# Optimization experiments

Hardware: AMD Instinct MI355X
Metric: run time of the kernel (lower is better)

## Reference

```python
import jax, jax.numpy as jnp
import numpy as np

EPS = 1e-08

def setup_inputs() -> dict:
    key = jax.random.key(0)
    ks = jax.random.split(key, 6)
    B, IN_C, OUT_C, H, W, STYLE_DIM = 16, 64, 64, 128, 128, 512
    x = jax.random.normal(ks[0], (B, IN_C, H, W), dtype=jnp.float32)
    style = jax.random.normal(ks[1], (B, STYLE_DIM), dtype=jnp.float32)
    # weight: (1, out_c, in_c, ks, ks) with kernel_size=1, kaiming-like scale
    fan_in = IN_C * 1 * 1
    gain = np.sqrt(2.0 / (1.0 + 0.2 ** 2))
    weight = jax.random.normal(ks[2], (1, OUT_C, IN_C, 1, 1), dtype=jnp.float32) * (gain / np.sqrt(fan_in))
    bias = jnp.zeros((1, OUT_C), dtype=jnp.float32)
    # geo_feature: Linear(style_dim, in_c)
    geo_w = jax.random.normal(ks[3], (IN_C, STYLE_DIM), dtype=jnp.float32) * (np.sqrt(2.0 / (1.0 + 0.2 ** 2)) / np.sqrt(STYLE_DIM))
    geo_b = jnp.zeros((IN_C,), dtype=jnp.float32)
    return {"x": x, "style": style, "weight": weight, "bias": bias, "geo_w": geo_w, "geo_b": geo_b}

def reference(x, style, weight, bias, geo_w, geo_b):
    # x: (b, in_c, h, w); style: (b, style_dim)
    # geo_feature linear -> (b, in_c), modulation factor (style + 1)
    s = style @ geo_w.T + geo_b                      # (b, in_c)
    mod = s + 1.0
    # per-sample modulated weight: (b, out_c, in_c, 1, 1) -> (b, out_c, in_c)
    w = weight[:, :, :, 0, 0] * mod[:, None, :]       # (b, out_c, in_c)
    # demodulate over (in_c, kh, kw)
    demod = jax.lax.rsqrt(jnp.sum(w * w, axis=2) + EPS)  # (b, out_c)
    w = w * demod[:, :, None]
    # groups=batch 1x1 conv == per-sample channel mixing
    out = jnp.einsum('boi,bihw->bohw', w, x)          # (b, out_c, h, w)
    out = out + bias[0][None, :, None, None]
    return out
```

## Files before the change

kernel.cpp:

```cpp
#include <hip/hip_runtime.h>
#include <hip/hip_bf16.h>

#define B_SZ 16
#define IN_C 64
#define OUT_C 64
#define STYLE_DIM 512
#define HW 16384
#define HWT 256
#define EPS 1e-8f

__global__ __launch_bounds__(256) void fused_kernel(
    const float* __restrict__ x,
    const float* __restrict__ style,
    const float* __restrict__ weight,
    const float* __restrict__ bias,
    const float* __restrict__ geo_w,
    const float* __restrict__ geo_b,
    float* __restrict__ out)
{
    __shared__ float smod[IN_C];
    __shared__ float sWT[IN_C * OUT_C];
    __shared__ float xs0[8][HWT];
    __shared__ float xs1[8][HWT];

    const int tid  = threadIdx.x;
    const int b    = blockIdx.x >> 6;
    const int hwt  = (blockIdx.x & 63) * HWT;
    const int wv   = tid >> 6;
    const int lane = tid & 63;

    const float* xg0 = x + ((size_t)b * IN_C + 2 * wv) * HW + hwt + lane * 4;

#define STAGE(CH, XS) do {                                                   \
        __builtin_amdgcn_global_load_lds(                                    \
            (const __attribute__((address_space(1))) void*)(xg0 + (size_t)(CH) * 8 * HW),        \
            (__attribute__((address_space(3))) void*)&(XS)[2 * wv][0], 16, 0, 0);                \
        __builtin_amdgcn_global_load_lds(                                    \
            (const __attribute__((address_space(1))) void*)(xg0 + ((size_t)(CH) * 8 + 1) * HW),  \
            (__attribute__((address_space(3))) void*)&(XS)[2 * wv + 1][0], 16, 0, 0);            \
    } while (0)

    STAGE(0, xs0);

    {
        const int i    = tid >> 2;
        const int part = tid & 3;
        const float4* st4 = reinterpret_cast<const float4*>(style + b * STYLE_DIM + part * 128);
        const float4* gw4 = reinterpret_cast<const float4*>(geo_w + i * STYLE_DIM + part * 128);
        float s = 0.0f;
        #pragma unroll
        for (int k = 0; k < 32; ++k) {
            const float4 a = st4[k];
            const float4 g = gw4[k];
            s = fmaf(a.x, g.x, s); s = fmaf(a.y, g.y, s);
            s = fmaf(a.z, g.z, s); s = fmaf(a.w, g.w, s);
        }
        s += __shfl_xor(s, 1);
        s += __shfl_xor(s, 2);
        if (part == 0) smod[i] = s + geo_b[i] + 1.0f;
    }
    __syncthreads();

    {
        const int o    = tid >> 2;
        const int part = tid & 3;
        const float* wr = weight + o * IN_C + part * 16;
        const float* sm = smod + part * 16;
        float wvv[16];
        float d = 0.0f;
        #pragma unroll
        for (int k = 0; k < 16; ++k) {
            wvv[k] = wr[k] * sm[k];
            d = fmaf(wvv[k], wvv[k], d);
        }
        d += __shfl_xor(d, 1);
        d += __shfl_xor(d, 2);
        d = rsqrtf(d + EPS);
        #pragma unroll
        for (int k = 0; k < 16; ++k)
            sWT[(part * 16 + k) * OUT_C + o] = wvv[k] * d;
    }
    __syncthreads();

    const int og  = (tid >> 5) * 8;
    const int hwg = (tid & 31) * 4;

    float acc[8][8];
    #pragma unroll
    for (int o = 0; o < 8; ++o)
        #pragma unroll
        for (int h = 0; h < 8; ++h) acc[o][h] = 0.0f;

#define COMPUTE_CHUNK(XS, C0) do {                                           \
        _Pragma("unroll")                                                    \
        for (int cc = 0; cc < 8; ++cc) {                                     \
            const float4 xa = *reinterpret_cast<const float4*>(&(XS)[cc][hwg]);        \
            const float4 xc = *reinterpret_cast<const float4*>(&(XS)[cc][128 + hwg]);  \
            const float4 w0 = *reinterpret_cast<const float4*>(&sWT[((C0) + cc) * OUT_C + og]);     \
            const float4 w1 = *reinterpret_cast<const float4*>(&sWT[((C0) + cc) * OUT_C + og + 4]); \
            const float wvv[8] = {w0.x, w0.y, w0.z, w0.w, w1.x, w1.y, w1.z, w1.w};     \
            const float xv[8]  = {xa.x, xa.y, xa.z, xa.w, xc.x, xc.y, xc.z, xc.w};     \
            _Pragma("unroll")                                                \
            for (int o = 0; o < 8; ++o)                                      \
                _Pragma("unroll")                                            \
                for (int h = 0; h < 8; ++h)                                  \
                    acc[o][h] = fmaf(wvv[o], xv[h], acc[o][h]);              \
        }                                                                    \
    } while (0)

    #pragma unroll
    for (int cp = 0; cp < 4; ++cp) {
        const int cA = 2 * cp, cB = 2 * cp + 1;
        STAGE(cB, xs1);
        COMPUTE_CHUNK(xs0, cA * 8);
        __syncthreads();
        if (cB < 7) STAGE(cB + 1, xs0);
        COMPUTE_CHUNK(xs1, cB * 8);
        if (cB < 7) __syncthreads();
    }
#undef COMPUTE_CHUNK
#undef STAGE

    float* ob = out + ((size_t)b * OUT_C + og) * HW + hwt;
    #pragma unroll
    for (int o = 0; o < 8; ++o) {
        const float bv = bias[og + o];
        float4 r0, r1;
        r0.x = acc[o][0] + bv;  r0.y = acc[o][1] + bv;
        r0.z = acc[o][2] + bv;  r0.w = acc[o][3] + bv;
        r1.x = acc[o][4] + bv;  r1.y = acc[o][5] + bv;
        r1.z = acc[o][6] + bv;  r1.w = acc[o][7] + bv;
        *reinterpret_cast<float4*>(ob + (size_t)o * HW + hwg)       = r0;
        *reinterpret_cast<float4*>(ob + (size_t)o * HW + 128 + hwg) = r1;
    }
}

extern "C" void kernel_launch(void* const* d_in, const int* in_sizes, int n_in,
                              void* d_out, int out_size, void* d_ws, size_t ws_size,
                              hipStream_t stream) {
    const float* x      = (const float*)d_in[0];
    const float* style  = (const float*)d_in[1];
    const float* weight = (const float*)d_in[2];
    const float* bias   = (const float*)d_in[3];
    const float* geo_w  = (const float*)d_in[4];
    const float* geo_b  = (const float*)d_in[5];
    float* out = (float*)d_out;

    fused_kernel<<<B_SZ * (HW / HWT), 256, 0, stream>>>(
        x, style, weight, bias, geo_w, geo_b, out);
}
```

Baseline: 152.8 us.

## Split weight modulation into separate kernel and stream x directly from global

Moves the per-sample modulated weight computation into a small precursor kernel that writes transposed weights to workspace. The conv kernel drops LDS staging and barriers, loading x directly with float2 prefetch and wave-uniform weights, with fewer accumulators per thread for higher occupancy. It adds a second launch, and the waves of each block re-read x through cache.

Measured after the change: 275.6 us. 1.8x slower.

```diff
diff --git a/kernel.cpp b/kernel.cpp
--- a/kernel.cpp
+++ b/kernel.cpp
@@ -6,41 +6,18 @@
 #define OUT_C 64
 #define STYLE_DIM 512
 #define HW 16384
-#define HWT 256
 #define EPS 1e-8f
 
-__global__ __launch_bounds__(256) void fused_kernel(
-    const float* __restrict__ x,
+__global__ __launch_bounds__(256) void modw_kernel(
     const float* __restrict__ style,
     const float* __restrict__ weight,
-    const float* __restrict__ bias,
     const float* __restrict__ geo_w,
     const float* __restrict__ geo_b,
-    float* __restrict__ out)
+    float* __restrict__ WT)
 {
+    const int b   = blockIdx.x;
+    const int tid = threadIdx.x;
     __shared__ float smod[IN_C];
-    __shared__ float sWT[IN_C * OUT_C];
-    __shared__ float xs0[8][HWT];
-    __shared__ float xs1[8][HWT];
-
-    const int tid  = threadIdx.x;
-    const int b    = blockIdx.x >> 6;
-    const int hwt  = (blockIdx.x & 63) * HWT;
-    const int wv   = tid >> 6;
-    const int lane = tid & 63;
-
-    const float* xg0 = x + ((size_t)b * IN_C + 2 * wv) * HW + hwt + lane * 4;
-
-#define STAGE(CH, XS) do {                                                   \
-        __builtin_amdgcn_global_load_lds(                                    \
-            (const __attribute__((address_space(1))) void*)(xg0 + (size_t)(CH) * 8 * HW),        \
-            (__attribute__((address_space(3))) void*)&(XS)[2 * wv][0], 16, 0, 0);                \
-        __builtin_amdgcn_global_load_lds(                                    \
-            (const __attribute__((address_space(1))) void*)(xg0 + ((size_t)(CH) * 8 + 1) * HW),  \
-            (__attribute__((address_space(3))) void*)&(XS)[2 * wv + 1][0], 16, 0, 0);            \
-    } while (0)
-
-    STAGE(0, xs0);
 
     {
         const int i    = tid >> 2;
@@ -66,72 +43,66 @@
         const int part = tid & 3;
         const float* wr = weight + o * IN_C + part * 16;
         const float* sm = smod + part * 16;
-        float wvv[16];
+        float wv[16];
         float d = 0.0f;
         #pragma unroll
         for (int k = 0; k < 16; ++k) {
-            wvv[k] = wr[k] * sm[k];
-            d = fmaf(wvv[k], wvv[k], d);
+            wv[k] = wr[k] * sm[k];
+            d = fmaf(wv[k], wv[k], d);
         }
         d += __shfl_xor(d, 1);
         d += __shfl_xor(d, 2);
         d = rsqrtf(d + EPS);
         #pragma unroll
         for (int k = 0; k < 16; ++k)
-            sWT[(part * 16 + k) * OUT_C + o] = wvv[k] * d;
+            WT[(b << 12) + (part * 16 + k) * OUT_C + o] = wv[k] * d;
     }
-    __syncthreads();
+}
 
-    const int og  = (tid >> 5) * 8;
-    const int hwg = (tid & 31) * 4;
+__global__ __launch_bounds__(256, 6) void conv_kernel(
+    const float* __restrict__ x,
+    const float* __restrict__ WT,
+    const float* __restrict__ bias,
+    float* __restrict__ out)
+{
+    const int tid  = threadIdx.x;
+    const int b    = blockIdx.x >> 7;
+    const int hw0  = (blockIdx.x & 127) << 7;
+    const int lane = tid & 63;
+    int og = (tid >> 6) << 4;
+    og = __builtin_amdgcn_readfirstlane(og);
 
-    float acc[8][8];
+    const float* wrow = WT + (b << 12) + og;
+    const float* xb   = x + (size_t)(b << 6) * HW + hw0 + (lane << 1);
+
+    float2 acc[16];
     #pragma unroll
-    for (int o = 0; o < 8; ++o)
-        #pragma unroll
-        for (int h = 0; h < 8; ++h) acc[o][h] = 0.0f;
+    for (int o = 0; o < 16; ++o) acc[o] = make_float2(0.0f, 0.0f);
 
-#define COMPUTE_CHUNK(XS, C0) do {                                           \
-        _Pragma("unroll")                                                    \
-        for (int cc = 0; cc < 8; ++cc) {                                     \
-            const float4 xa = *reinterpret_cast<const float4*>(&(XS)[cc][hwg]);        \
-            const float4 xc = *reinterpret_cast<const float4*>(&(XS)[cc][128 + hwg]);  \
-            const float4 w0 = *reinterpret_cast<const float4*>(&sWT[((C0) + cc) * OUT_C + og]);     \
-            const float4 w1 = *reinterpret_cast<const float4*>(&sWT[((C0) + cc) * OUT_C + og + 4]); \
-            const float wvv[8] = {w0.x, w0.y, w0.z, w0.w, w1.x, w1.y, w1.z, w1.w};     \
-            const float xv[8]  = {xa.x, xa.y, xa.z, xa.w, xc.x, xc.y, xc.z, xc.w};     \
-            _Pragma("unroll")                                                \
-            for (int o = 0; o < 8; ++o)                                      \
-                _Pragma("unroll")                                            \
-                for (int h = 0; h < 8; ++h)                                  \
-                    acc[o][h] = fmaf(wvv[o], xv[h], acc[o][h]);              \
-        }                                                                    \
-    } while (0)
+    float2 x0 = *reinterpret_cast<const float2*>(xb);
+    float2 x1 = *reinterpret_cast<const float2*>(xb + HW);
 
     #pragma unroll
-    for (int cp = 0; cp < 4; ++cp) {
-        const int cA = 2 * cp, cB = 2 * cp + 1;
-        STAGE(cB, xs1);
-        COMPUTE_CHUNK(xs0, cA * 8);
-        __syncthreads();
-        if (cB < 7) STAGE(cB + 1, xs0);
-        COMPUTE_CHUNK(xs1, cB * 8);
-        if (cB < 7) __syncthreads();
+    for (int i = 0; i < IN_C; ++i) {
+        float2 xn = x1;
+        if (i + 2 < IN_C)
+            xn = *reinterpret_cast<const float2*>(xb + (size_t)(i + 2) * HW);
+        const float* wr = wrow + (i << 6);
+        #pragma unroll
+        for (int o = 0; o < 16; ++o) {
+            const float w = wr[o];
+            acc[o].x = fmaf(w, x0.x, acc[o].x);
+            acc[o].y = fmaf(w, x0.y, acc[o].y);
+        }
+        x0 = x1; x1 = xn;
     }
-#undef COMPUTE_CHUNK
-#undef STAGE
 
-    float* ob = out + ((size_t)b * OUT_C + og) * HW + hwt;
+    float* ob = out + (size_t)((b << 6) + og) * HW + hw0 + (lane << 1);
     #pragma unroll
-    for (int o = 0; o < 8; ++o) {
+    for (int o = 0; o < 16; ++o) {
         const float bv = bias[og + o];
-        float4 r0, r1;
-        r0.x = acc[o][0] + bv;  r0.y = acc[o][1] + bv;
-        r0.z = acc[o][2] + bv;  r0.w = acc[o][3] + bv;
-        r1.x = acc[o][4] + bv;  r1.y = acc[o][5] + bv;
-        r1.z = acc[o][6] + bv;  r1.w = acc[o][7] + bv;
-        *reinterpret_cast<float4*>(ob + (size_t)o * HW + hwg)       = r0;
-        *reinterpret_cast<float4*>(ob + (size_t)o * HW + 128 + hwg) = r1;
+        const float2 r = make_float2(acc[o].x + bv, acc[o].y + bv);
+        *reinterpret_cast<float2*>(ob + (size_t)o * HW) = r;
     }
 }
 
@@ -145,7 +116,8 @@
     const float* geo_w  = (const float*)d_in[4];
     const float* geo_b  = (const float*)d_in[5];
     float* out = (float*)d_out;
+    float* WT  = (float*)d_ws;
 
-    fused_kernel<<<B_SZ * (HW / HWT), 256, 0, stream>>>(
-        x, style, weight, bias, geo_w, geo_b, out);
+    modw_kernel<<<B_SZ, 256, 0, stream>>>(style, weight, geo_w, geo_b, WT);
+    conv_kernel<<<B_SZ * (HW / 128), 256, 0, stream>>>(x, WT, bias, out);
 }
```
